# Optimization experiments

Hardware: AMD Instinct MI355X
Metric: run time of the kernel (lower is better)

Reference implementation:

```python
import jax, jax.numpy as jnp
import numpy as np

D_MODEL = 1024
NUM_HEADS = 16
D_K = D_MODEL // NUM_HEADS


def setup_inputs() -> dict:
    key = jax.random.key(0)
    ks = jax.random.split(key, 11)
    B, S = 2, 2048
    s = 1.0 / np.sqrt(D_MODEL)
    inp = {
        'q': jax.random.normal(ks[0], (B, S, D_MODEL), jnp.float32),
        'k': jax.random.normal(ks[1], (B, S, D_MODEL), jnp.float32),
        'v': jax.random.normal(ks[2], (B, S, D_MODEL), jnp.float32),
        'w_q': jax.random.normal(ks[3], (D_MODEL, D_MODEL), jnp.float32) * s,
        'b_q': jnp.zeros((D_MODEL,), jnp.float32),
        'w_k': jax.random.normal(ks[4], (D_MODEL, D_MODEL), jnp.float32) * s,
        'b_k': jnp.zeros((D_MODEL,), jnp.float32),
        'w_v': jax.random.normal(ks[5], (D_MODEL, D_MODEL), jnp.float32) * s,
        'b_v': jnp.zeros((D_MODEL,), jnp.float32),
        'w_o': jax.random.normal(ks[6], (D_MODEL, D_MODEL), jnp.float32) * s,
        'b_o': jnp.zeros((D_MODEL,), jnp.float32),
    }
    return inp


def reference(q, k, v, w_q, b_q, w_k, b_k, w_v, b_v, w_o, b_o):
    B, S, _ = q.shape
    # linear projections (torch Linear: x @ W.T + b)
    def proj(x, w, b):
        y = x @ w.T + b
        # [B, S, D] -> [B, H, S, d_k]
        return y.reshape(B, -1, NUM_HEADS, D_K).transpose(0, 2, 1, 3)

    Q = proj(q, w_q, b_q)
    K = proj(k, w_k, b_k)
    V = proj(v, w_v, b_v)

    scale = 1.0 / np.sqrt(D_K).astype(np.float32)
    scores = jnp.einsum('bhqd,bhkd->bhqk', Q, K) * scale  # [B,H,S,S]
    weights = jax.nn.softmax(scores, axis=-1)
    # dropout is identity in eval mode
    x = jnp.einsum('bhqk,bhkd->bhqd', weights, V)
    x = x.transpose(0, 2, 1, 3).reshape(B, S, NUM_HEADS * D_K)
    return x @ w_o.T + b_o
```

## Files before the change

kernel.cpp:

```cpp
#include <hip/hip_runtime.h>

typedef __attribute__((ext_vector_type(8))) short short8;
typedef __attribute__((ext_vector_type(4))) float f32x4;

#define NHEADS 16
#define DK 64
#define SEQ 2048
#define DMODEL 1024

__device__ __forceinline__ unsigned short f2bf(float f) {
  union { float f; unsigned int u; } c; c.f = f;
  unsigned int u = c.u;
  return (unsigned short)((u + 0x7FFFu + ((u >> 16) & 1u)) >> 16);
}

__device__ __forceinline__ float exp2_hw(float x) {
  float y;
  asm("v_exp_f32 %0, %1" : "=v"(y) : "v"(x));
  return y;
}

__device__ __forceinline__ unsigned int cvtpk_bf16(float lo, float hi) {
  unsigned int r;
  asm("v_cvt_pk_bf16_f32 %0, %1, %2" : "=v"(r) : "v"(lo), "v"(hi));
  return r;
}

__device__ __forceinline__ short8 ldg16(const unsigned short* p) {
  return *reinterpret_cast<const short8*>(p);
}

__device__ __forceinline__ void gload_lds16(const unsigned short* g, unsigned short* l) {
  __builtin_amdgcn_global_load_lds(
      (const __attribute__((address_space(1))) unsigned int*)g,
      (__attribute__((address_space(3))) unsigned int*)l, 16, 0, 0);
}

__global__ void cast_qkv(const float* __restrict__ a0, const float* __restrict__ a1,
                         const float* __restrict__ a2, unsigned short* __restrict__ d0,
                         unsigned short* __restrict__ d1, unsigned short* __restrict__ d2) {
  const float* s = blockIdx.y == 0 ? a0 : (blockIdx.y == 1 ? a1 : a2);
  unsigned short* d = blockIdx.y == 0 ? d0 : (blockIdx.y == 1 ? d1 : d2);
  int i = blockIdx.x * blockDim.x + threadIdx.x;
  float4 v = reinterpret_cast<const float4*>(s)[i];
  ushort4 o;
  o.x = f2bf(v.x); o.y = f2bf(v.y); o.z = f2bf(v.z); o.w = f2bf(v.w);
  reinterpret_cast<ushort4*>(d)[i] = o;
}

__global__ void cast_w4(const float* __restrict__ a0, const float* __restrict__ a1,
                        const float* __restrict__ a2, const float* __restrict__ a3,
                        unsigned short* __restrict__ d0, unsigned short* __restrict__ d1,
                        unsigned short* __restrict__ d2, unsigned short* __restrict__ d3) {
  const float* s = blockIdx.y == 0 ? a0 : (blockIdx.y == 1 ? a1 : (blockIdx.y == 2 ? a2 : a3));
  unsigned short* d = blockIdx.y == 0 ? d0 : (blockIdx.y == 1 ? d1 : (blockIdx.y == 2 ? d2 : d3));
  int i = blockIdx.x * blockDim.x + threadIdx.x;
  float4 v = reinterpret_cast<const float4*>(s)[i];
  ushort4 o;
  o.x = f2bf(v.x); o.y = f2bf(v.y); o.z = f2bf(v.z); o.w = f2bf(v.w);
  reinterpret_cast<ushort4*>(d)[i] = o;
}

struct ProjPtrs {
  const unsigned short* A0; const unsigned short* A1; const unsigned short* A2;
  const unsigned short* W0; const unsigned short* W1; const unsigned short* W2;
  const float* bias0; const float* bias1; const float* bias2;
  unsigned short* dst0; unsigned short* dst1; unsigned short* dst2;
};

__global__ __launch_bounds__(256) void gemm_proj(ProjPtrs p) {
  __shared__ __align__(16) unsigned short As[2][4096];
  __shared__ __align__(16) unsigned short Bs[2][4096];
  const int mode = blockIdx.z;
  const unsigned short* A = mode == 0 ? p.A0 : (mode == 1 ? p.A1 : p.A2);
  const unsigned short* W = mode == 0 ? p.W0 : (mode == 1 ? p.W1 : p.W2);
  const float* bias = mode == 0 ? p.bias0 : (mode == 1 ? p.bias1 : p.bias2);
  unsigned short* dst = mode == 0 ? p.dst0 : (mode == 1 ? p.dst1 : p.dst2);
  const int m0 = blockIdx.y * 128, n0 = blockIdx.x * 128;
  const int t = threadIdx.x, lane = t & 63, w = t >> 6;
  const int wr = w >> 1, wc = w & 1;
  const int lr = lane >> 4, lc = lane & 15;
  const unsigned short* a_src0 = A + (size_t)(m0 + (t >> 2)) * DMODEL + (t & 3) * 8;
  const unsigned short* a_src1 = A + (size_t)(m0 + 64 + (t >> 2)) * DMODEL + (t & 3) * 8;
  const unsigned short* w_src0 = W + (size_t)(n0 + (t >> 2)) * DMODEL + (t & 3) * 8;
  const unsigned short* w_src1 = W + (size_t)(n0 + 64 + (t >> 2)) * DMODEL + (t & 3) * 8;

  f32x4 acc[4][4] = {};
  gload_lds16(a_src0, &As[0][t * 8]);
  gload_lds16(a_src1, &As[0][2048 + t * 8]);
  gload_lds16(w_src0, &Bs[0][t * 8]);
  gload_lds16(w_src1, &Bs[0][2048 + t * 8]);
  __syncthreads();
  int buf = 0;
  for (int k0 = 0; k0 < DMODEL; k0 += 32) {
    if (k0 < DMODEL - 32) {
      const int kn = k0 + 32;
      gload_lds16(a_src0 + kn, &As[buf ^ 1][t * 8]);
      gload_lds16(a_src1 + kn, &As[buf ^ 1][2048 + t * 8]);
      gload_lds16(w_src0 + kn, &Bs[buf ^ 1][t * 8]);
      gload_lds16(w_src1 + kn, &Bs[buf ^ 1][2048 + t * 8]);
    }
    short8 a[4], b[4];
#pragma unroll
    for (int i = 0; i < 4; ++i) {
      a[i] = *reinterpret_cast<const short8*>(&As[buf][(wr * 64 + i * 16 + lc) * 32 + lr * 8]);
      b[i] = *reinterpret_cast<const short8*>(&Bs[buf][(wc * 64 + i * 16 + lc) * 32 + lr * 8]);
    }
#pragma unroll
    for (int mi = 0; mi < 4; ++mi)
#pragma unroll
      for (int ni = 0; ni < 4; ++ni)
        acc[mi][ni] = __builtin_amdgcn_mfma_f32_16x16x32_bf16(a[mi], b[ni], acc[mi][ni], 0, 0, 0);
    __syncthreads();
    buf ^= 1;
  }
#pragma unroll
  for (int mi = 0; mi < 4; ++mi) {
#pragma unroll
    for (int ni = 0; ni < 4; ++ni) {
      const int cg = n0 + wc * 64 + ni * 16 + lc;
      const int rb = m0 + wr * 64 + mi * 16 + lr * 4;
      const float bv = bias[cg];
      const int h = cg >> 6, d = cg & 63;
      if (mode == 2) {
        const int bb = rb >> 11, s = rb & 2047;
        ushort4 pk;
        pk.x = f2bf(acc[mi][ni][0] + bv);
        pk.y = f2bf(acc[mi][ni][1] + bv);
        pk.z = f2bf(acc[mi][ni][2] + bv);
        pk.w = f2bf(acc[mi][ni][3] + bv);
        *reinterpret_cast<ushort4*>(dst + (((size_t)((bb * NHEADS + h) * DK + d)) << 11) + s) = pk;
      } else {
        const float sc = (mode == 0) ? 0.18033688f : 1.0f;
#pragma unroll
        for (int j = 0; j < 4; ++j) {
          const int rg = rb + j;
          const int bb = rg >> 11, s = rg & 2047;
          dst[((size_t)(bb * NHEADS + h) * SEQ + s) * DK + d] = f2bf((acc[mi][ni][j] + bv) * sc);
        }
      }
    }
  }
}

__global__ __launch_bounds__(256) void gemm_out(const unsigned short* __restrict__ A,
                                                const unsigned short* __restrict__ W,
                                                const float* __restrict__ bias,
                                                float* __restrict__ out) {
  __shared__ __align__(16) unsigned short As[2][4096];
  __shared__ __align__(16) unsigned short Bs[2][2048];
  const int m0 = blockIdx.y * 128, n0 = blockIdx.x * 64;
  const int t = threadIdx.x, lane = t & 63, w = t >> 6;
  const int wr = w >> 1, wc = w & 1;
  const int lr = lane >> 4, lc = lane & 15;
  const unsigned short* a_src0 = A + (size_t)(m0 + (t >> 2)) * DMODEL + (t & 3) * 8;
  const unsigned short* a_src1 = A + (size_t)(m0 + 64 + (t >> 2)) * DMODEL + (t & 3) * 8;
  const unsigned short* w_src0 = W + (size_t)(n0 + (t >> 2)) * DMODEL + (t & 3) * 8;

  f32x4 acc[4][2] = {};
  gload_lds16(a_src0, &As[0][t * 8]);
  gload_lds16(a_src1, &As[0][2048 + t * 8]);
  gload_lds16(w_src0, &Bs[0][t * 8]);
  __syncthreads();
  int buf = 0;
  for (int k0 = 0; k0 < DMODEL; k0 += 32) {
    if (k0 < DMODEL - 32) {
      const int kn = k0 + 32;
      gload_lds16(a_src0 + kn, &As[buf ^ 1][t * 8]);
      gload_lds16(a_src1 + kn, &As[buf ^ 1][2048 + t * 8]);
      gload_lds16(w_src0 + kn, &Bs[buf ^ 1][t * 8]);
    }
    short8 a[4], b[2];
#pragma unroll
    for (int i = 0; i < 4; ++i)
      a[i] = *reinterpret_cast<const short8*>(&As[buf][(wr * 64 + i * 16 + lc) * 32 + lr * 8]);
#pragma unroll
    for (int i = 0; i < 2; ++i)
      b[i] = *reinterpret_cast<const short8*>(&Bs[buf][(wc * 32 + i * 16 + lc) * 32 + lr * 8]);
#pragma unroll
    for (int mi = 0; mi < 4; ++mi)
#pragma unroll
      for (int ni = 0; ni < 2; ++ni)
        acc[mi][ni] = __builtin_amdgcn_mfma_f32_16x16x32_bf16(a[mi], b[ni], acc[mi][ni], 0, 0, 0);
    __syncthreads();
    buf ^= 1;
  }
#pragma unroll
  for (int mi = 0; mi < 4; ++mi)
#pragma unroll
    for (int ni = 0; ni < 2; ++ni) {
      const int cg = n0 + wc * 32 + ni * 16 + lc;
      const int rb = m0 + wr * 64 + mi * 16 + lr * 4;
      const float bv = bias[cg];
#pragma unroll
      for (int j = 0; j < 4; ++j)
        out[(size_t)(rb + j) * DMODEL + cg] = acc[mi][ni][j] + bv;
    }
}

__global__ __launch_bounds__(256) void attn_fwd(const unsigned short* __restrict__ Qh,
                                                const unsigned short* __restrict__ Kh,
                                                const unsigned short* __restrict__ Vt,
                                                unsigned short* __restrict__ Oh) {
  __shared__ __align__(16) unsigned short Ktile[2][4096];
  __shared__ __align__(16) unsigned short Vtile[2][4096];
  __shared__ __align__(16) unsigned short P[4][32][76];
  const int t = threadIdx.x, w = t >> 6, lane = t & 63;
  const int bx = ((blockIdx.x & 7) << 6) | (blockIdx.x >> 3);
  const int bh = bx >> 4, qblk = bx & 15;
  const int q0 = qblk * 128 + w * 32;
  const unsigned short* Qp = Qh + (size_t)bh * SEQ * DK;
  const unsigned short* Kp = Kh + (size_t)bh * SEQ * DK;
  const unsigned short* Vp = Vt + (size_t)bh * DK * SEQ;
  const int r = lane & 15, g = lane >> 4;

  const short8 qa0 = ldg16(Qp + (size_t)(q0 + r) * DK + g * 8);
  const short8 qa1 = ldg16(Qp + (size_t)(q0 + r) * DK + 32 + g * 8);
  const short8 qb0 = ldg16(Qp + (size_t)(q0 + 16 + r) * DK + g * 8);
  const short8 qb1 = ldg16(Qp + (size_t)(q0 + 16 + r) * DK + 32 + g * 8);

  const int c0 = w * 64 + lane, c1 = c0 + 256;
  const int r0 = c0 >> 3, s0 = (c0 & 7) ^ (r0 & 7);
  const int r1 = c1 >> 3, s1 = (c1 & 7) ^ (r1 & 7);
  const unsigned short* ks0 = Kp + r0 * DK + s0 * 8;
  const unsigned short* ks1 = Kp + r1 * DK + s1 * 8;
  const unsigned short* vs0 = Vp + (size_t)r0 * SEQ + s0 * 8;
  const unsigned short* vs1 = Vp + (size_t)r1 * SEQ + s1 * 8;

  float mA = -1e30f, lA = 0.f, mB = -1e30f, lB = 0.f;
  f32x4 oA[4] = {}, oB[4] = {};

  const int sw0 = ((g ^ (r & 7)) << 3);
  const int sw1 = (((g + 4) ^ (r & 7)) << 3);
  char* prowA = (char*)&P[w][r][0];
  char* prowB = (char*)&P[w][16 + r][0];

  gload_lds16(ks0, &Ktile[0][w * 512]);
  gload_lds16(ks1, &Ktile[0][2048 + w * 512]);
  gload_lds16(vs0, &Vtile[0][w * 512]);
  gload_lds16(vs1, &Vtile[0][2048 + w * 512]);
  __syncthreads();

  int buf = 0;
  for (int kt = 0; kt < 32; ++kt) {
    if (kt < 31) {
      const int kvn = (kt + 1) * 64;
      gload_lds16(ks0 + kvn * DK, &Ktile[buf ^ 1][w * 512]);
      gload_lds16(ks1 + kvn * DK, &Ktile[buf ^ 1][2048 + w * 512]);
      gload_lds16(vs0 + kvn, &Vtile[buf ^ 1][w * 512]);
      gload_lds16(vs1 + kvn, &Vtile[buf ^ 1][2048 + w * 512]);
    }
    f32x4 sA[4] = {}, sB[4] = {};
    __builtin_amdgcn_s_setprio(1);
#pragma unroll
    for (int nt = 0; nt < 4; ++nt) {
      const short8 k0 = *reinterpret_cast<const short8*>(&Ktile[buf][(nt * 16 + r) * 64 + sw0]);
      const short8 k1 = *reinterpret_cast<const short8*>(&Ktile[buf][(nt * 16 + r) * 64 + sw1]);
      sA[nt] = __builtin_amdgcn_mfma_f32_16x16x32_bf16(k0, qa0, sA[nt], 0, 0, 0);
      sA[nt] = __builtin_amdgcn_mfma_f32_16x16x32_bf16(k1, qa1, sA[nt], 0, 0, 0);
      sB[nt] = __builtin_amdgcn_mfma_f32_16x16x32_bf16(k0, qb0, sB[nt], 0, 0, 0);
      sB[nt] = __builtin_amdgcn_mfma_f32_16x16x32_bf16(k1, qb1, sB[nt], 0, 0, 0);
    }
    __builtin_amdgcn_s_setprio(0);
    {
      f32x4 pm;
#pragma unroll
      for (int j = 0; j < 4; ++j)
        pm[j] = fmaxf(fmaxf(sA[0][j], sA[1][j]), fmaxf(sA[2][j], sA[3][j]));
      float pmax = fmaxf(fmaxf(pm[0], pm[1]), fmaxf(pm[2], pm[3]));
      pmax = fmaxf(pmax, __shfl_xor(pmax, 16));
      pmax = fmaxf(pmax, __shfl_xor(pmax, 32));
      if (!__all(pmax - mA <= 8.f)) {
        const float mn = fmaxf(mA, pmax);
        const float al = exp2_hw(mA - mn);
        mA = mn; lA *= al;
        float alj[4];
#pragma unroll
        for (int j = 0; j < 4; ++j) alj[j] = __shfl(al, 4 * g + j, 16);
#pragma unroll
        for (int nt = 0; nt < 4; ++nt)
#pragma unroll
          for (int j = 0; j < 4; ++j) oA[nt][j] *= alj[j];
      }
#pragma unroll
      for (int nt = 0; nt < 4; ++nt)
#pragma unroll
        for (int j = 0; j < 4; ++j) sA[nt][j] = exp2_hw(sA[nt][j] - mA);
      f32x4 s4;
#pragma unroll
      for (int j = 0; j < 4; ++j) s4[j] = (sA[0][j] + sA[1][j]) + (sA[2][j] + sA[3][j]);
      float sum = (s4[0] + s4[1]) + (s4[2] + s4[3]);
      sum += __shfl_xor(sum, 16);
      sum += __shfl_xor(sum, 32);
      lA += sum;
#pragma unroll
      for (int nt = 0; nt < 4; ++nt) {
        uint2 pk;
        pk.x = cvtpk_bf16(sA[nt][0], sA[nt][1]);
        pk.y = cvtpk_bf16(sA[nt][2], sA[nt][3]);
        *reinterpret_cast<uint2*>(prowA + nt * 32 + g * 8) = pk;
      }
    }
    {
      f32x4 pm;
#pragma unroll
      for (int j = 0; j < 4; ++j)
        pm[j] = fmaxf(fmaxf(sB[0][j], sB[1][j]), fmaxf(sB[2][j], sB[3][j]));
      float pmax = fmaxf(fmaxf(pm[0], pm[1]), fmaxf(pm[2], pm[3]));
      pmax = fmaxf(pmax, __shfl_xor(pmax, 16));
      pmax = fmaxf(pmax, __shfl_xor(pmax, 32));
      if (!__all(pmax - mB <= 8.f)) {
        const float mn = fmaxf(mB, pmax);
        const float al = exp2_hw(mB - mn);
        mB = mn; lB *= al;
        float alj[4];
#pragma unroll
        for (int j = 0; j < 4; ++j) alj[j] = __shfl(al, 4 * g + j, 16);
#pragma unroll
        for (int nt = 0; nt < 4; ++nt)
#pragma unroll
          for (int j = 0; j < 4; ++j) oB[nt][j] *= alj[j];
      }
#pragma unroll
      for (int nt = 0; nt < 4; ++nt)
#pragma unroll
        for (int j = 0; j < 4; ++j) sB[nt][j] = exp2_hw(sB[nt][j] - mB);
      f32x4 s4;
#pragma unroll
      for (int j = 0; j < 4; ++j) s4[j] = (sB[0][j] + sB[1][j]) + (sB[2][j] + sB[3][j]);
      float sum = (s4[0] + s4[1]) + (s4[2] + s4[3]);
      sum += __shfl_xor(sum, 16);
      sum += __shfl_xor(sum, 32);
      lB += sum;
#pragma unroll
      for (int nt = 0; nt < 4; ++nt) {
        uint2 pk;
        pk.x = cvtpk_bf16(sB[nt][0], sB[nt][1]);
        pk.y = cvtpk_bf16(sB[nt][2], sB[nt][3]);
        *reinterpret_cast<uint2*>(prowB + nt * 32 + g * 8) = pk;
      }
    }
    union { short8 v; unsigned long long q[2]; } pA0, pA1, pB0, pB1;
    pA0.q[0] = *reinterpret_cast<const unsigned long long*>(prowA + g * 16);
    pA0.q[1] = *reinterpret_cast<const unsigned long long*>(prowA + g * 16 + 8);
    pA1.q[0] = *reinterpret_cast<const unsigned long long*>(prowA + 64 + g * 16);
    pA1.q[1] = *reinterpret_cast<const unsigned long long*>(prowA + 64 + g * 16 + 8);
    pB0.q[0] = *reinterpret_cast<const unsigned long long*>(prowB + g * 16);
    pB0.q[1] = *reinterpret_cast<const unsigned long long*>(prowB + g * 16 + 8);
    pB1.q[0] = *reinterpret_cast<const unsigned long long*>(prowB + 64 + g * 16);
    pB1.q[1] = *reinterpret_cast<const unsigned long long*>(prowB + 64 + g * 16 + 8);
    __builtin_amdgcn_s_setprio(1);
#pragma unroll
    for (int nt = 0; nt < 4; ++nt) {
      const short8 v0 = *reinterpret_cast<const short8*>(&Vtile[buf][(nt * 16 + r) * 64 + sw0]);
      const short8 v1 = *reinterpret_cast<const short8*>(&Vtile[buf][(nt * 16 + r) * 64 + sw1]);
      oA[nt] = __builtin_amdgcn_mfma_f32_16x16x32_bf16(pA0.v, v0, oA[nt], 0, 0, 0);
      oA[nt] = __builtin_amdgcn_mfma_f32_16x16x32_bf16(pA1.v, v1, oA[nt], 0, 0, 0);
      oB[nt] = __builtin_amdgcn_mfma_f32_16x16x32_bf16(pB0.v, v0, oB[nt], 0, 0, 0);
      oB[nt] = __builtin_amdgcn_mfma_f32_16x16x32_bf16(pB1.v, v1, oB[nt], 0, 0, 0);
    }
    __builtin_amdgcn_s_setprio(0);
    __syncthreads();
    buf ^= 1;
  }

  const float invA = 1.f / lA, invB = 1.f / lB;
  float ivA[4], ivB[4];
#pragma unroll
  for (int j = 0; j < 4; ++j) {
    ivA[j] = __shfl(invA, 4 * g + j, 16);
    ivB[j] = __shfl(invB, 4 * g + j, 16);
  }
  const size_t ob = ((size_t)((bh >> 4) * SEQ + q0)) * DMODEL + (size_t)(bh & 15) * DK;
#pragma unroll
  for (int nt = 0; nt < 4; ++nt)
#pragma unroll
    for (int j = 0; j < 4; ++j) {
      Oh[ob + (size_t)(g * 4 + j) * DMODEL + nt * 16 + r] = f2bf(oA[nt][j] * ivA[j]);
      Oh[ob + (size_t)(16 + g * 4 + j) * DMODEL + nt * 16 + r] = f2bf(oB[nt][j] * ivB[j]);
    }
}

extern "C" void kernel_launch(void* const* d_in, const int* in_sizes, int n_in,
                              void* d_out, int out_size, void* d_ws, size_t ws_size,
                              hipStream_t stream) {
  const float* q   = (const float*)d_in[0];
  const float* k   = (const float*)d_in[1];
  const float* v   = (const float*)d_in[2];
  const float* w_q = (const float*)d_in[3];
  const float* b_q = (const float*)d_in[4];
  const float* w_k = (const float*)d_in[5];
  const float* b_k = (const float*)d_in[6];
  const float* w_v = (const float*)d_in[7];
  const float* b_v = (const float*)d_in[8];
  const float* w_o = (const float*)d_in[9];
  const float* b_o = (const float*)d_in[10];
  float* out = (float*)d_out;
  char* ws = (char*)d_ws;
  const size_t MB = (size_t)1 << 20;
  unsigned short* qc  = (unsigned short*)(ws + 0 * MB);
  unsigned short* kc  = (unsigned short*)(ws + 8 * MB);
  unsigned short* vc  = (unsigned short*)(ws + 16 * MB);
  unsigned short* wqc = (unsigned short*)(ws + 24 * MB);
  unsigned short* wkc = (unsigned short*)(ws + 26 * MB);
  unsigned short* wvc = (unsigned short*)(ws + 28 * MB);
  unsigned short* woc = (unsigned short*)(ws + 30 * MB);
  unsigned short* Qh  = (unsigned short*)(ws + 32 * MB);
  unsigned short* Kh  = (unsigned short*)(ws + 40 * MB);
  unsigned short* Vt  = (unsigned short*)(ws + 48 * MB);
  unsigned short* Oh  = (unsigned short*)(ws + 56 * MB);

  cast_qkv<<<dim3(4096, 3), 256, 0, stream>>>(q, k, v, qc, kc, vc);
  cast_w4<<<dim3(1024, 4), 256, 0, stream>>>(w_q, w_k, w_v, w_o, wqc, wkc, wvc, woc);

  ProjPtrs p;
  p.A0 = qc; p.A1 = kc; p.A2 = vc;
  p.W0 = wqc; p.W1 = wkc; p.W2 = wvc;
  p.bias0 = b_q; p.bias1 = b_k; p.bias2 = b_v;
  p.dst0 = Qh; p.dst1 = Kh; p.dst2 = Vt;
  gemm_proj<<<dim3(8, 32, 3), 256, 0, stream>>>(p);

  attn_fwd<<<512, 256, 0, stream>>>(Qh, Kh, Vt, Oh);

  gemm_out<<<dim3(16, 32), 256, 0, stream>>>(Oh, woc, b_o, out);
}
```

Before: 252.4 us.

## Triple-buffer GEMM K-loops with vmcnt waits, merge cast kernels, stage V transpose via LDS

```diff
diff --git a/kernel.cpp b/kernel.cpp
--- a/kernel.cpp
+++ b/kernel.cpp
@@ -36,25 +36,24 @@
       (__attribute__((address_space(3))) unsigned int*)l, 16, 0, 0);
 }
 
-__global__ void cast_qkv(const float* __restrict__ a0, const float* __restrict__ a1,
-                         const float* __restrict__ a2, unsigned short* __restrict__ d0,
-                         unsigned short* __restrict__ d1, unsigned short* __restrict__ d2) {
-  const float* s = blockIdx.y == 0 ? a0 : (blockIdx.y == 1 ? a1 : a2);
-  unsigned short* d = blockIdx.y == 0 ? d0 : (blockIdx.y == 1 ? d1 : d2);
-  int i = blockIdx.x * blockDim.x + threadIdx.x;
-  float4 v = reinterpret_cast<const float4*>(s)[i];
-  ushort4 o;
-  o.x = f2bf(v.x); o.y = f2bf(v.y); o.z = f2bf(v.z); o.w = f2bf(v.w);
-  reinterpret_cast<ushort4*>(d)[i] = o;
-}
-
-__global__ void cast_w4(const float* __restrict__ a0, const float* __restrict__ a1,
-                        const float* __restrict__ a2, const float* __restrict__ a3,
-                        unsigned short* __restrict__ d0, unsigned short* __restrict__ d1,
-                        unsigned short* __restrict__ d2, unsigned short* __restrict__ d3) {
-  const float* s = blockIdx.y == 0 ? a0 : (blockIdx.y == 1 ? a1 : (blockIdx.y == 2 ? a2 : a3));
-  unsigned short* d = blockIdx.y == 0 ? d0 : (blockIdx.y == 1 ? d1 : (blockIdx.y == 2 ? d2 : d3));
-  int i = blockIdx.x * blockDim.x + threadIdx.x;
+struct CastPtrs {
+  const float* s0; const float* s1; const float* s2; const float* s3;
+  const float* s4; const float* s5; const float* s6;
+  unsigned short* d0; unsigned short* d1; unsigned short* d2; unsigned short* d3;
+  unsigned short* d4; unsigned short* d5; unsigned short* d6;
+};
+
+__global__ void cast_all(CastPtrs c) {
+  const int b = blockIdx.x;
+  const float* s; unsigned short* d; int off;
+  if (b < 4096)        { s = c.s0; d = c.d0; off = b; }
+  else if (b < 8192)   { s = c.s1; d = c.d1; off = b - 4096; }
+  else if (b < 12288)  { s = c.s2; d = c.d2; off = b - 8192; }
+  else if (b < 13312)  { s = c.s3; d = c.d3; off = b - 12288; }
+  else if (b < 14336)  { s = c.s4; d = c.d4; off = b - 13312; }
+  else if (b < 15360)  { s = c.s5; d = c.d5; off = b - 14336; }
+  else                 { s = c.s6; d = c.d6; off = b - 15360; }
+  const int i = off * 256 + threadIdx.x;
   float4 v = reinterpret_cast<const float4*>(s)[i];
   ushort4 o;
   o.x = f2bf(v.x); o.y = f2bf(v.y); o.z = f2bf(v.z); o.w = f2bf(v.w);
@@ -69,8 +68,7 @@
 };
 
 __global__ __launch_bounds__(256) void gemm_proj(ProjPtrs p) {
-  __shared__ __align__(16) unsigned short As[2][4096];
-  __shared__ __align__(16) unsigned short Bs[2][4096];
+  __shared__ __align__(16) unsigned short S[24576];
   const int mode = blockIdx.z;
   const unsigned short* A = mode == 0 ? p.A0 : (mode == 1 ? p.A1 : p.A2);
   const unsigned short* W = mode == 0 ? p.W0 : (mode == 1 ? p.W1 : p.W2);
@@ -81,57 +79,93 @@
   const int wr = w >> 1, wc = w & 1;
   const int lr = lane >> 4, lc = lane & 15;
   const unsigned short* a_src0 = A + (size_t)(m0 + (t >> 2)) * DMODEL + (t & 3) * 8;
-  const unsigned short* a_src1 = A + (size_t)(m0 + 64 + (t >> 2)) * DMODEL + (t & 3) * 8;
+  const unsigned short* a_src1 = a_src0 + (size_t)64 * DMODEL;
   const unsigned short* w_src0 = W + (size_t)(n0 + (t >> 2)) * DMODEL + (t & 3) * 8;
-  const unsigned short* w_src1 = W + (size_t)(n0 + 64 + (t >> 2)) * DMODEL + (t & 3) * 8;
+  const unsigned short* w_src1 = w_src0 + (size_t)64 * DMODEL;
 
   f32x4 acc[4][4] = {};
-  gload_lds16(a_src0, &As[0][t * 8]);
-  gload_lds16(a_src1, &As[0][2048 + t * 8]);
-  gload_lds16(w_src0, &Bs[0][t * 8]);
-  gload_lds16(w_src1, &Bs[0][2048 + t * 8]);
-  __syncthreads();
-  int buf = 0;
-  for (int k0 = 0; k0 < DMODEL; k0 += 32) {
-    if (k0 < DMODEL - 32) {
-      const int kn = k0 + 32;
-      gload_lds16(a_src0 + kn, &As[buf ^ 1][t * 8]);
-      gload_lds16(a_src1 + kn, &As[buf ^ 1][2048 + t * 8]);
-      gload_lds16(w_src0 + kn, &Bs[buf ^ 1][t * 8]);
-      gload_lds16(w_src1 + kn, &Bs[buf ^ 1][2048 + t * 8]);
-    }
+
+#define PSTAGE(s, bi) do { \
+    gload_lds16(a_src0 + (s) * 32, S + (bi) * 4096 + t * 8); \
+    gload_lds16(a_src1 + (s) * 32, S + (bi) * 4096 + 2048 + t * 8); \
+    gload_lds16(w_src0 + (s) * 32, S + 12288 + (bi) * 4096 + t * 8); \
+    gload_lds16(w_src1 + (s) * 32, S + 12288 + (bi) * 4096 + 2048 + t * 8); } while (0)
+
+  auto compute = [&](const int bi) {
+    const unsigned short* Ab = S + bi * 4096;
+    const unsigned short* Bb = S + 12288 + bi * 4096;
     short8 a[4], b[4];
 #pragma unroll
     for (int i = 0; i < 4; ++i) {
-      a[i] = *reinterpret_cast<const short8*>(&As[buf][(wr * 64 + i * 16 + lc) * 32 + lr * 8]);
-      b[i] = *reinterpret_cast<const short8*>(&Bs[buf][(wc * 64 + i * 16 + lc) * 32 + lr * 8]);
+      a[i] = *reinterpret_cast<const short8*>(Ab + (wr * 64 + i * 16 + lc) * 32 + lr * 8);
+      b[i] = *reinterpret_cast<const short8*>(Bb + (wc * 64 + i * 16 + lc) * 32 + lr * 8);
     }
 #pragma unroll
     for (int mi = 0; mi < 4; ++mi)
 #pragma unroll
       for (int ni = 0; ni < 4; ++ni)
         acc[mi][ni] = __builtin_amdgcn_mfma_f32_16x16x32_bf16(a[mi], b[ni], acc[mi][ni], 0, 0, 0);
+  };
+
+  PSTAGE(0, 0);
+  PSTAGE(1, 1);
+  for (int k = 0; k < 30; ++k) {
+    PSTAGE(k + 2, (k + 2) % 3);
+    asm volatile("s_waitcnt vmcnt(8)" ::: "memory");
+    __builtin_amdgcn_s_barrier();
+    __builtin_amdgcn_sched_barrier(0);
+    compute(k % 3);
+    __builtin_amdgcn_sched_barrier(0);
+    __builtin_amdgcn_s_barrier();
+    __builtin_amdgcn_sched_barrier(0);
+  }
+  asm volatile("s_waitcnt vmcnt(4)" ::: "memory");
+  __builtin_amdgcn_s_barrier();
+  __builtin_amdgcn_sched_barrier(0);
+  compute(0);
+  __builtin_amdgcn_sched_barrier(0);
+  __builtin_amdgcn_s_barrier();
+  __builtin_amdgcn_sched_barrier(0);
+  asm volatile("s_waitcnt vmcnt(0)" ::: "memory");
+  __builtin_amdgcn_s_barrier();
+  __builtin_amdgcn_sched_barrier(0);
+  compute(1);
+
+  if (mode == 2) {
     __syncthreads();
-    buf ^= 1;
-  }
-#pragma unroll
-  for (int mi = 0; mi < 4; ++mi) {
-#pragma unroll
-    for (int ni = 0; ni < 4; ++ni) {
-      const int cg = n0 + wc * 64 + ni * 16 + lc;
-      const int rb = m0 + wr * 64 + mi * 16 + lr * 4;
-      const float bv = bias[cg];
-      const int h = cg >> 6, d = cg & 63;
-      if (mode == 2) {
-        const int bb = rb >> 11, s = rb & 2047;
-        ushort4 pk;
-        pk.x = f2bf(acc[mi][ni][0] + bv);
-        pk.y = f2bf(acc[mi][ni][1] + bv);
-        pk.z = f2bf(acc[mi][ni][2] + bv);
-        pk.w = f2bf(acc[mi][ni][3] + bv);
-        *reinterpret_cast<ushort4*>(dst + (((size_t)((bb * NHEADS + h) * DK + d)) << 11) + s) = pk;
-      } else {
-        const float sc = (mode == 0) ? 0.18033688f : 1.0f;
+    unsigned short* T = S + w * 4608;
+    const int h = (n0 + wc * 64) >> 6;
+    const int rb0 = m0 + wr * 64;
+    const int bb = rb0 >> 11, s_base = rb0 & 2047;
+#pragma unroll
+    for (int mi = 0; mi < 4; ++mi) {
+#pragma unroll
+      for (int ni = 0; ni < 4; ++ni) {
+        const float bv = bias[n0 + wc * 64 + ni * 16 + lc];
+        uint2 pk;
+        pk.x = cvtpk_bf16(acc[mi][ni][0] + bv, acc[mi][ni][1] + bv);
+        pk.y = cvtpk_bf16(acc[mi][ni][2] + bv, acc[mi][ni][3] + bv);
+        *reinterpret_cast<uint2*>(&T[(ni * 16 + lc) * 72 + mi * 16 + lr * 4]) = pk;
+      }
+    }
+    __builtin_amdgcn_sched_barrier(0);
+    unsigned short* dstb = dst + ((size_t)(bb * NHEADS + h) * 64) * 2048 + s_base;
+#pragma unroll
+    for (int i = 0; i < 8; ++i) {
+      const int drow = i * 8 + (lane >> 3), scol = (lane & 7) * 8;
+      const short8 val = *reinterpret_cast<const short8*>(&T[drow * 72 + scol]);
+      *reinterpret_cast<short8*>(dstb + (size_t)drow * 2048 + scol) = val;
+    }
+  } else {
+    const float sc = (mode == 0) ? 0.18033688f : 1.0f;
+#pragma unroll
+    for (int mi = 0; mi < 4; ++mi) {
+#pragma unroll
+      for (int ni = 0; ni < 4; ++ni) {
+        const int cg = n0 + wc * 64 + ni * 16 + lc;
+        const int rb = m0 + wr * 64 + mi * 16 + lr * 4;
+        const float bv = bias[cg];
+        const int h = cg >> 6, d = cg & 63;
 #pragma unroll
         for (int j = 0; j < 4; ++j) {
           const int rg = rb + j;
@@ -147,44 +181,63 @@
                                                 const unsigned short* __restrict__ W,
                                                 const float* __restrict__ bias,
                                                 float* __restrict__ out) {
-  __shared__ __align__(16) unsigned short As[2][4096];
-  __shared__ __align__(16) unsigned short Bs[2][2048];
+  __shared__ __align__(16) unsigned short S[18432];
   const int m0 = blockIdx.y * 128, n0 = blockIdx.x * 64;
   const int t = threadIdx.x, lane = t & 63, w = t >> 6;
   const int wr = w >> 1, wc = w & 1;
   const int lr = lane >> 4, lc = lane & 15;
   const unsigned short* a_src0 = A + (size_t)(m0 + (t >> 2)) * DMODEL + (t & 3) * 8;
-  const unsigned short* a_src1 = A + (size_t)(m0 + 64 + (t >> 2)) * DMODEL + (t & 3) * 8;
+  const unsigned short* a_src1 = a_src0 + (size_t)64 * DMODEL;
   const unsigned short* w_src0 = W + (size_t)(n0 + (t >> 2)) * DMODEL + (t & 3) * 8;
 
   f32x4 acc[4][2] = {};
-  gload_lds16(a_src0, &As[0][t * 8]);
-  gload_lds16(a_src1, &As[0][2048 + t * 8]);
-  gload_lds16(w_src0, &Bs[0][t * 8]);
-  __syncthreads();
-  int buf = 0;
-  for (int k0 = 0; k0 < DMODEL; k0 += 32) {
-    if (k0 < DMODEL - 32) {
-      const int kn = k0 + 32;
-      gload_lds16(a_src0 + kn, &As[buf ^ 1][t * 8]);
-      gload_lds16(a_src1 + kn, &As[buf ^ 1][2048 + t * 8]);
-      gload_lds16(w_src0 + kn, &Bs[buf ^ 1][t * 8]);
-    }
+
+#define OSTAGE(s, bi) do { \
+    gload_lds16(a_src0 + (s) * 32, S + (bi) * 4096 + t * 8); \
+    gload_lds16(a_src1 + (s) * 32, S + (bi) * 4096 + 2048 + t * 8); \
+    gload_lds16(w_src0 + (s) * 32, S + 12288 + (bi) * 2048 + t * 8); } while (0)
+
+  auto compute = [&](const int bi) {
+    const unsigned short* Ab = S + bi * 4096;
+    const unsigned short* Bb = S + 12288 + bi * 2048;
     short8 a[4], b[2];
 #pragma unroll
     for (int i = 0; i < 4; ++i)
-      a[i] = *reinterpret_cast<const short8*>(&As[buf][(wr * 64 + i * 16 + lc) * 32 + lr * 8]);
+      a[i] = *reinterpret_cast<const short8*>(Ab + (wr * 64 + i * 16 + lc) * 32 + lr * 8);
 #pragma unroll
     for (int i = 0; i < 2; ++i)
-      b[i] = *reinterpret_cast<const short8*>(&Bs[buf][(wc * 32 + i * 16 + lc) * 32 + lr * 8]);
+      b[i] = *reinterpret_cast<const short8*>(Bb + (wc * 32 + i * 16 + lc) * 32 + lr * 8);
 #pragma unroll
     for (int mi = 0; mi < 4; ++mi)
 #pragma unroll
       for (int ni = 0; ni < 2; ++ni)
         acc[mi][ni] = __builtin_amdgcn_mfma_f32_16x16x32_bf16(a[mi], b[ni], acc[mi][ni], 0, 0, 0);
-    __syncthreads();
-    buf ^= 1;
+  };
+
+  OSTAGE(0, 0);
+  OSTAGE(1, 1);
+  for (int k = 0; k < 30; ++k) {
+    OSTAGE(k + 2, (k + 2) % 3);
+    asm volatile("s_waitcnt vmcnt(6)" ::: "memory");
+    __builtin_amdgcn_s_barrier();
+    __builtin_amdgcn_sched_barrier(0);
+    compute(k % 3);
+    __builtin_amdgcn_sched_barrier(0);
+    __builtin_amdgcn_s_barrier();
+    __builtin_amdgcn_sched_barrier(0);
   }
+  asm volatile("s_waitcnt vmcnt(3)" ::: "memory");
+  __builtin_amdgcn_s_barrier();
+  __builtin_amdgcn_sched_barrier(0);
+  compute(0);
+  __builtin_amdgcn_sched_barrier(0);
+  __builtin_amdgcn_s_barrier();
+  __builtin_amdgcn_sched_barrier(0);
+  asm volatile("s_waitcnt vmcnt(0)" ::: "memory");
+  __builtin_amdgcn_s_barrier();
+  __builtin_amdgcn_sched_barrier(0);
+  compute(1);
+
 #pragma unroll
   for (int mi = 0; mi < 4; ++mi)
 #pragma unroll
@@ -410,8 +463,10 @@
   unsigned short* Vt  = (unsigned short*)(ws + 48 * MB);
   unsigned short* Oh  = (unsigned short*)(ws + 56 * MB);
 
-  cast_qkv<<<dim3(4096, 3), 256, 0, stream>>>(q, k, v, qc, kc, vc);
-  cast_w4<<<dim3(1024, 4), 256, 0, stream>>>(w_q, w_k, w_v, w_o, wqc, wkc, wvc, woc);
+  CastPtrs cp;
+  cp.s0 = q; cp.s1 = k; cp.s2 = v; cp.s3 = w_q; cp.s4 = w_k; cp.s5 = w_v; cp.s6 = w_o;
+  cp.d0 = qc; cp.d1 = kc; cp.d2 = vc; cp.d3 = wqc; cp.d4 = wkc; cp.d5 = wvc; cp.d6 = woc;
+  cast_all<<<16384, 256, 0, stream>>>(cp);
 
   ProjPtrs p;
   p.A0 = qc; p.A1 = kc; p.A2 = vc;
```

New measurement: 240.5 us. 1.05x faster.
